# Performance work log

Hardware: AMD Instinct MI355X
Metric: run time of the kernel (lower is better)

Reference implementation:

```python
import jax, jax.numpy as jnp
import numpy as np

NODE, HIDDEN, BATCH, OUT, BUF = 200, 10, 50, 64, 500
DT = 0.0001
# ParamsJR('JR') defaults (all variances 0 -> constants, not Parameters)
A_, a_, B_, b_ = 3.25, 100.0, 22.0, 50.0
g_, c1_, c2_, c3_, c4_ = 1000.0, 135.0, 135.0 * 0.8, 135.0 * 0.25, 135.0 * 0.25
std_in_, vmax, v0, r_, y0, cy0 = 100.0, 5.0, 6.0, 0.56, 2.0, 5.0
LB, U_UB, NOISE_LB, SAT = 0.01, 500.0, 150.0, 1000.0


def setup_inputs() -> dict:
    key = jax.random.key(0)
    ks = jax.random.split(key, 8)
    inp = jax.random.normal(ks[0], (NODE, HIDDEN, BATCH), dtype=jnp.float32)
    noise_in = jax.random.normal(ks[1], (NODE, HIDDEN, BATCH), dtype=jnp.float32)
    hx = jax.random.uniform(ks[2], (NODE, 6), dtype=jnp.float32)
    hE = jax.random.uniform(ks[3], (NODE, BUF), dtype=jnp.float32)
    sc = jax.random.uniform(ks[4], (NODE, NODE), dtype=jnp.float32)
    w_bb = jax.random.uniform(ks[5], (NODE, NODE), dtype=jnp.float32)  # fitted gains (init 0.05 in torch)
    lm = jax.random.normal(ks[6], (OUT, NODE), dtype=jnp.float32)  # lead-field
    delays = jax.random.randint(ks[7], (NODE, NODE), 0, BUF)  # (dist/(1.5+relu(mu))).int64
    return {"inp": inp, "noise_in": noise_in, "hx": hx, "hE": hE,
            "sc": sc, "w_bb": w_bb, "lm": lm, "delays": delays}


def _sigmoid(x):
    return vmax / (1.0 + jnp.exp(r_ * (v0 - x)))


def _sys2nd(A, a, u, x, v):
    return A * a * u - 2.0 * a * v - a * a * x


def _forward(inp, noise_in, hx, hE, sc, w_bb, lm, delays):
    relu = jax.nn.relu
    A_e, a_e = relu(A_), 1.0 + relu(a_)          # 0*con+relu(A), 1*con+relu(a)
    B_e, b_e = relu(B_), 1.0 + relu(b_)
    g_e, c1e, c2e, c3e, c4e = (LB + relu(g_), LB + relu(c1_), LB + relu(c2_),
                               LB + relu(c3_), LB + relu(c4_))
    std_e = NOISE_LB + relu(std_in_)

    # normalized laplacian-style connectivity
    w = jnp.exp(w_bb) * sc
    wl = jnp.log1p(0.5 * (w + w.T))
    w_n = wl / jnp.linalg.norm(wl)
    dg = -jnp.diag(jnp.sum(w_n, axis=1))          # (node, node)
    rows = jnp.arange(NODE)[:, None]

    def step(carry, xs):
        M, E, I, Mv, Ev, Iv, hEb = carry
        u, noise = xs                              # (node,1) each
        Ed = hEb[rows, delays]                     # Ed[i,j] = hE[i, delays[i,j]]
        LEd = jnp.sum(w_n * Ed.T, axis=1, keepdims=True)  # (node,1)
        rM = _sigmoid(E - I)
        rE = (std_e * noise + g_e * (LEd + dg @ E)
              + c2e * _sigmoid(c1e * M))
        rI = c4e * _sigmoid(c3e * M)
        ddM = M + DT * Mv
        ddE = E + DT * Ev
        ddI = I + DT * Iv
        ddMv = Mv + DT * _sys2nd(A_e, a_e, u + U_UB * jnp.tanh(rM / U_UB), M, Mv)
        ddEv = Ev + DT * _sys2nd(A_e, a_e, U_UB * jnp.tanh(rE / U_UB), E, Ev)
        ddIv = Iv + DT * _sys2nd(B_e, b_e, U_UB * jnp.tanh(rI / U_UB), I, Iv)
        sat = lambda x: SAT * jnp.tanh(x / SAT)
        M, E, I, Mv, Ev, Iv = (sat(ddM), sat(ddE), sat(ddI),
                               sat(ddMv), sat(ddEv), sat(ddIv))
        hEb = jnp.concatenate([M, hEb[:, :-1]], axis=1)  # push pyramidal state into delay buffer
        return (M, E, I, Mv, Ev, Iv, hEb), None

    def tr_step(carry, xs):
        u_tr, n_tr = xs                            # (hidden, node, 1)
        carry, _ = jax.lax.scan(step, carry, (u_tr, n_tr))
        M, E, I, Mv, Ev, Iv, _ = carry
        return carry, (M[:, 0], E[:, 0], I[:, 0], Mv[:, 0], Ev[:, 0], Iv[:, 0])

    M, E, I = hx[:, 0:1], hx[:, 1:2], hx[:, 2:3]
    Mv, Ev, Iv = hx[:, 3:4], hx[:, 4:5], hx[:, 5:6]
    u_all = jnp.transpose(inp, (2, 1, 0))[..., None]       # (batch, hidden, node, 1)
    n_all = jnp.transpose(noise_in, (2, 1, 0))[..., None]
    carry, recs = jax.lax.scan(tr_step, (M, E, I, Mv, Ev, Iv, hE), (u_all, n_all))
    Mb, Eb, Ib, Mvb, Evb, Ivb = recs                       # (batch, node) each

    # lead-field: row-normalize then remove channel mean
    lm_n = lm / jnp.sqrt(jnp.sum(lm ** 2, axis=1, keepdims=True))
    lm_t = lm_n - jnp.mean(lm_n, axis=0, keepdims=True)
    eeg = cy0 * jnp.einsum('on,bn->ob', lm_t, Eb - Ib) - y0  # (output, batch)

    M, E, I, Mv, Ev, Iv, hEb = carry
    current_state = jnp.concatenate([M, E, I, Mv, Ev, Iv], axis=1)
    return eeg, current_state, Eb.T, Ib.T, Mb.T, Evb.T, Ivb.T, Mvb.T, hEb


def reference(inp, noise_in, hx, hE, sc, w_bb, lm, delays):
    return _forward(inp, noise_in, hx, hE, sc, w_bb, lm, delays)
```

## Files before the change

### kernel.cpp

```cpp
#include <hip/hip_runtime.h>
#include <math.h>

#define N_NODE 200
#define RING   512
#define ROWF   545
#define NSTEP  500
#define TB     32
#define NB     16
#define NWG    8
#define NTHR   256
#define JSL    25
#define NEARCAP 32
#define MDEP   36

#define FPBUF   (NWG * N_NODE * TB)
#define OFF_FP  0
#define OFF_BAR (2 * FPBUF)
#define WS_NEED ((size_t)(2 * FPBUF + 64) * 4)

#define SM_RED   0
#define SM_MREC  64
#define SM_NOFF  28864
#define SM_NW    54464
#define SM_LED   80864
#define SM_RING  106464
#define SM_TOTAL 160964
#define SM_LMT   64
#define SM_DIFF  51264

__device__ __forceinline__ float sigm(float x) {
    return 5.0f / (1.0f + expf(0.56f * (6.0f - x)));
}
__device__ __forceinline__ float satf(float x) {
    return 1000.0f * tanhf(x / 1000.0f);
}

__device__ __forceinline__ void grid_barrier(int* slot, int nwg) {
    __syncthreads();
    if (threadIdx.x == 0) {
        __threadfence();
        __hip_atomic_fetch_add(slot, 1, __ATOMIC_ACQ_REL, __HIP_MEMORY_SCOPE_AGENT);
        while (__hip_atomic_load(slot, __ATOMIC_ACQUIRE, __HIP_MEMORY_SCOPE_AGENT) < nwg) {
            __builtin_amdgcn_s_sleep(2);
        }
        __threadfence();
    }
    __syncthreads();
}

__global__ void zero_bar(int* bar) {
    if (threadIdx.x < 64) bar[threadIdx.x] = 0;
}

__global__ __launch_bounds__(NTHR, 1)
void jansen_reg(const float* __restrict__ inp, const float* __restrict__ noise_in,
                const float* __restrict__ hx,  const float* __restrict__ hE,
                const float* __restrict__ sc,  const float* __restrict__ wbb,
                const float* __restrict__ lm,  const int*   __restrict__ delays,
                float* __restrict__ out, float* __restrict__ ws)
{
    __shared__ char smem[SM_TOTAL];
    double*   red  = (double*)(smem + SM_RED);
    float*    Mrec = (float*)(smem + SM_MREC);
    unsigned* nOFF = (unsigned*)(smem + SM_NOFF);
    float*    nW   = (float*)(smem + SM_NW);
    float*    LEdS = (float*)(smem + SM_LED);
    float*    ringS= (float*)(smem + SM_RING);

    const int tid = threadIdx.x;
    const int wg  = blockIdx.x;
    const int i   = tid;
    const int jlo = wg * JSL;

    float* fp  = ws + OFF_FP;
    int*   bar = (int*)(ws + OFF_BAR);

    double ssq = 0.0;
    for (int q = tid; q < N_NODE * N_NODE; q += NTHR) {
        int j = q / N_NODE, ii = q - j * N_NODE;
        float w1 = expf(wbb[ii * N_NODE + j]) * sc[ii * N_NODE + j];
        float w2 = expf(wbb[j * N_NODE + ii]) * sc[j * N_NODE + ii];
        float wl = log1pf(0.5f * (w1 + w2));
        ssq += (double)wl * (double)wl;
    }
    #pragma unroll
    for (int off = 32; off > 0; off >>= 1) ssq += __shfl_down(ssq, off, 64);
    if ((tid & 63) == 0) red[tid >> 6] = ssq;

    for (int p = tid; p < JSL * ROWF; p += NTHR) {
        int jl = p / ROWF, x = p - jl * ROWF;
        float v = 0.0f;
        if (x < 544) {
            int dd = (x < RING) ? (511 - x) : (1023 - x);
            if (dd < 500) v = hE[(jlo + jl) * 500 + dd];
        }
        ringS[p] = v;
    }
    for (int p = tid; p < MDEP * N_NODE; p += NTHR) {
        int s = p / N_NODE, j = p - s * N_NODE;
        Mrec[p] = (s >= 4) ? hE[j * 500 + (35 - s)] : 0.0f;
    }
    for (int p = tid; p < NEARCAP * N_NODE; p += NTHR) {
        nOFF[p] = 0u;
        nW[p]   = 0.0f;
    }
    __syncthreads();
    if (tid == 0) {
        double s = 0.0;
        #pragma unroll
        for (int r = 0; r < 8; ++r) s += red[r];
        red[0] = 1.0 / sqrt(s);
    }
    __syncthreads();
    const float inv = (float)red[0];

    float rowsum = 0.0f;
    float M = 0, E = 0, I = 0, Mvv = 0, Evv = 0, Ivv = 0;
    float wreg[JSL];
    int   ereg[JSL];
    #pragma unroll
    for (int jl = 0; jl < JSL; ++jl) { wreg[jl] = 0.0f; ereg[jl] = 0; }
    if (i < N_NODE) {
        int cnt = 0;
        for (int j = 0; j < N_NODE; ++j) {
            float w1 = expf(wbb[i * N_NODE + j]) * sc[i * N_NODE + j];
            float w2 = expf(wbb[j * N_NODE + i]) * sc[j * N_NODE + i];
            float w  = log1pf(0.5f * (w1 + w2)) * inv;
            int d = delays[j * N_NODE + i];
            rowsum += w;
            if (d < NEARCAP && cnt < NEARCAP) {
                nOFF[cnt * N_NODE + i] = (unsigned)((35 - d) * N_NODE + j);
                nW  [cnt * N_NODE + i] = w;
                ++cnt;
            }
        }
        #pragma unroll
        for (int jl = 0; jl < JSL; ++jl) {
            int j = jlo + jl;
            float w1 = expf(wbb[i * N_NODE + j]) * sc[i * N_NODE + j];
            float w2 = expf(wbb[j * N_NODE + i]) * sc[j * N_NODE + i];
            float w  = log1pf(0.5f * (w1 + w2)) * inv;
            int d = delays[j * N_NODE + i];
            wreg[jl] = (d < NEARCAP) ? 0.0f : w;
            ereg[jl] = 511 - d;
        }
        M   = hx[i * 6 + 0]; E   = hx[i * 6 + 1]; I   = hx[i * 6 + 2];
        Mvv = hx[i * 6 + 3]; Evv = hx[i * 6 + 4]; Ivv = hx[i * 6 + 5];
    }

    int   noffR[NEARCAP];
    float nwR[NEARCAP];
    {
        const int ii = (i < N_NODE) ? i : 0;
        #pragma unroll
        for (int n = 0; n < NEARCAP; ++n) {
            noffR[n] = (int)nOFF[n * N_NODE + ii];
            nwR[n]   = nW[n * N_NODE + ii];
        }
    }
    __syncthreads();

    for (int b = 0; b < NB; ++b) {
        const int t0 = b * TB;
        float* fpb = fp + (b & 1) * FPBUF;

        float u0=0, u1=0, u2=0, n0=0, n1=0, n2=0;

        if (i < N_NODE) {
            float ac[TB];
            #pragma unroll
            for (int k = 0; k < TB; ++k) ac[k] = 0.0f;
            #pragma unroll
            for (int jl = 0; jl < JSL; ++jl) {
                float w  = wreg[jl];
                int   p0 = (t0 + ereg[jl]) & 511;
                const float* rb = ringS + jl * ROWF + p0;
                #pragma unroll
                for (int k = 0; k < TB; ++k)
                    ac[k] = fmaf(w, rb[k], ac[k]);
            }
            float4* fpw = (float4*)(fpb + wg * (N_NODE * TB) + i * TB);
            #pragma unroll
            for (int q = 0; q < 8; ++q)
                fpw[q] = make_float4(ac[4*q+0], ac[4*q+1], ac[4*q+2], ac[4*q+3]);

            {
                int ta = t0, tb2 = t0 + 1, tc = t0 + 2;
                int ba = ta / 10,  ha = ta  - 10 * ba;
                int bbq = tb2 / 10, hb = tb2 - 10 * bbq;
                int bc = tc / 10,  hc = tc  - 10 * bc;
                u0 = inp     [i * 500 + ha * 50 + ba];
                n0 = noise_in[i * 500 + ha * 50 + ba];
                u1 = inp     [i * 500 + hb * 50 + bbq];
                n1 = noise_in[i * 500 + hb * 50 + bbq];
                u2 = inp     [i * 500 + hc * 50 + bc];
                n2 = noise_in[i * 500 + hc * 50 + bc];
            }
        }

        grid_barrier(bar + b, NWG);

        if (i < N_NODE) {
            const float* basep = fpb + i * TB;
            #pragma unroll
            for (int c = 0; c < 8; ++c) {
                float sx = 0, sy = 0, sz = 0, sw = 0;
                #pragma unroll
                for (int g = 0; g < NWG; ++g) {
                    float4 q = *(const float4*)(basep + g * (N_NODE * TB) + c * 4);
                    sx += q.x; sy += q.y; sz += q.z; sw += q.w;
                }
                LEdS[(c * 4 + 0) * N_NODE + i] = sx;
                LEdS[(c * 4 + 1) * N_NODE + i] = sy;
                LEdS[(c * 4 + 2) * N_NODE + i] = sz;
                LEdS[(c * 4 + 3) * N_NODE + i] = sw;
            }
        }
        __syncthreads();

        const int kmax = (NSTEP - t0 < TB) ? (NSTEP - t0) : TB;
        int s36 = t0 % MDEP;
        int t3  = t0 + 3;
        int bb3 = t3 / 10, hh3 = t3 - 10 * bb3;
        int bcur = t0 / 10, hcur = t0 - 10 * bcur;
        const bool ringw = (i >= jlo) && (i < jlo + JSL);
        const int  rbase = (i - jlo) * ROWF;
        for (int k = 0; k < kmax; ++k) {
            const int t = t0 + k;
            if (i < N_NODE) {
                float LEd = LEdS[k * N_NODE + i];
                const int base36 = s36 * N_NODE;
                #pragma unroll
                for (int n = 0; n < NEARCAP; ++n) {
                    int addr = base36 + noffR[n];
                    if (addr >= MDEP * N_NODE) addr -= MDEP * N_NODE;
                    LEd = fmaf(nwR[n], Mrec[addr], LEd);
                }
                float u  = u0;
                float nz = n0;
                float rM = sigm(E - I);
                float rE = 250.0f * nz + 1000.01f * (LEd - rowsum * E) + 108.01f * sigm(135.01f * M);
                float rI = 33.76f * sigm(33.76f * M);
                float ddM = M + 1e-4f * Mvv;
                float ddE = E + 1e-4f * Evv;
                float ddI = I + 1e-4f * Ivv;
                float uu  = u + 500.0f * tanhf(rM / 500.0f);
                float ddMv = Mvv + 1e-4f * (328.25f * uu - 202.0f * Mvv - 10201.0f * M);
                float uE  = 500.0f * tanhf(rE / 500.0f);
                float ddEv = Evv + 1e-4f * (328.25f * uE - 202.0f * Evv - 10201.0f * E);
                float uI  = 500.0f * tanhf(rI / 500.0f);
                float ddIv = Ivv + 1e-4f * (1122.0f * uI - 102.0f * Ivv - 2601.0f * I);
                M   = satf(ddM);  E   = satf(ddE);  I   = satf(ddI);
                Mvv = satf(ddMv); Evv = satf(ddEv); Ivv = satf(ddIv);
                Mrec[s36 * N_NODE + i] = M;
                if (ringw) {
                    int pt = t & 511;
                    ringS[rbase + pt] = M;
                    if (pt < 32) ringS[rbase + pt + 512] = M;
                }
                if (wg == 0 && hcur == 9) {
                    out[ 4400 + i * 50 + bcur] = E;
                    out[14400 + i * 50 + bcur] = I;
                    out[24400 + i * 50 + bcur] = M;
                    out[34400 + i * 50 + bcur] = Evv;
                    out[44400 + i * 50 + bcur] = Ivv;
                    out[54400 + i * 50 + bcur] = Mvv;
                }
                u0 = u1; u1 = u2; n0 = n1; n1 = n2;
                if (t3 < NSTEP) {
                    u2 = inp     [i * 500 + hh3 * 50 + bb3];
                    n2 = noise_in[i * 500 + hh3 * 50 + bb3];
                }
                ++t3; ++hh3; if (hh3 == 10) { hh3 = 0; ++bb3; }
                ++hcur; if (hcur == 10) { hcur = 0; ++bcur; }
                ++s36; if (s36 == MDEP) s36 = 0;
            }
            __syncthreads();
        }
    }

    for (int p = tid; p < JSL * 500; p += NTHR) {
        int jl = p / 500, dd = p - jl * 500;
        out[64400 + (jlo + jl) * 500 + dd] = ringS[jl * ROWF + ((499 - dd) & 511)];
    }
    if (wg != 0) return;

    if (i < N_NODE) {
        out[3200 + i * 6 + 0] = M;
        out[3200 + i * 6 + 1] = E;
        out[3200 + i * 6 + 2] = I;
        out[3200 + i * 6 + 3] = Mvv;
        out[3200 + i * 6 + 4] = Evv;
        out[3200 + i * 6 + 5] = Ivv;
    }

    float* lmt  = (float*)(smem + SM_LMT);
    float* diff = (float*)(smem + SM_DIFF);
    __syncthreads();
    if (tid < 64) {
        float s = 0.0f;
        for (int n = 0; n < N_NODE; ++n) { float v = lm[tid * N_NODE + n]; s += v * v; }
        float ivn = 1.0f / sqrtf(s);
        for (int n = 0; n < N_NODE; ++n) lmt[tid * N_NODE + n] = lm[tid * N_NODE + n] * ivn;
    }
    __syncthreads();
    if (tid < N_NODE) {
        float s = 0.0f;
        for (int o = 0; o < 64; ++o) s += lmt[o * N_NODE + tid];
        s *= (1.0f / 64.0f);
        for (int o = 0; o < 64; ++o) lmt[o * N_NODE + tid] -= s;
    }
    __syncthreads();
    for (int p = tid; p < 10000; p += NTHR) diff[p] = out[4400 + p] - out[14400 + p];
    __syncthreads();
    for (int p = tid; p < 3200; p += NTHR) {
        int o = p / 50, bb = p - o * 50;
        float s = 0.0f;
        for (int n = 0; n < N_NODE; ++n)
            s = fmaf(lmt[o * N_NODE + n], diff[n * 50 + bb], s);
        out[p] = 5.0f * s - 2.0f;
    }
}

__global__ __launch_bounds__(1024, 1)
void jansen_main(const float* __restrict__ inp, const float* __restrict__ noise_in,
                 const float* __restrict__ hx,  const float* __restrict__ hE,
                 const float* __restrict__ sc,  const float* __restrict__ wbb,
                 const float* __restrict__ lm,  const int*   __restrict__ delays,
                 float* __restrict__ out, float* __restrict__ ws)
{
    const int tid = threadIdx.x;
    const int i   = tid & 255;
    const int c   = tid >> 8;

    float* ring = ws;
    float* lmt  = ws + N_NODE * RING;

    __shared__ double red[18];
    __shared__ float  part[4][N_NODE];
    __shared__ float  wn[N_NODE * N_NODE];

    double ssq = 0.0;
    for (int p = tid; p < N_NODE * N_NODE; p += 1024) {
        int r0 = p / N_NODE;
        int cc = p - r0 * N_NODE;
        float w1 = expf(wbb[p]) * sc[p];
        float w2 = expf(wbb[cc * N_NODE + r0]) * sc[cc * N_NODE + r0];
        float v  = log1pf(0.5f * (w1 + w2));
        wn[p] = v;
        ssq += (double)v * (double)v;
    }
    #pragma unroll
    for (int off = 32; off > 0; off >>= 1) ssq += __shfl_down(ssq, off, 64);
    if ((tid & 63) == 0) red[tid >> 6] = ssq;
    __syncthreads();
    if (tid == 0) {
        double s = 0.0;
        for (int k = 0; k < 16; ++k) s += red[k];
        red[16] = 1.0 / sqrt(s);
    }
    __syncthreads();
    const float inv_norm = (float)red[16];
    for (int p = tid; p < N_NODE * N_NODE; p += 1024) wn[p] *= inv_norm;

    for (int p = tid; p < N_NODE * 500; p += 1024) {
        int j = p / 500, dd = p - j * 500;
        ring[j * RING + (511 - dd)] = hE[p];
    }
    if (tid < 64) {
        float s = 0.0f;
        for (int n = 0; n < N_NODE; ++n) { float v = lm[tid * N_NODE + n]; s += v * v; }
        float inv = 1.0f / sqrtf(s);
        for (int n = 0; n < N_NODE; ++n) lmt[tid * N_NODE + n] = lm[tid * N_NODE + n] * inv;
    }
    __syncthreads();
    if (tid < N_NODE) {
        float s = 0.0f;
        for (int o = 0; o < 64; ++o) s += lmt[o * N_NODE + tid];
        s *= (1.0f / 64.0f);
        for (int o = 0; o < 64; ++o) lmt[o * N_NODE + tid] -= s;
    }

    unsigned int dpk[25];
    if (i < N_NODE) {
        #pragma unroll
        for (int r0 = 0; r0 < 25; ++r0) {
            int d0 = delays[(c * 50 + 2 * r0    ) * N_NODE + i];
            int d1 = delays[(c * 50 + 2 * r0 + 1) * N_NODE + i];
            unsigned e0 = (unsigned)((-1 - d0) & 511);
            unsigned e1 = (unsigned)((-1 - d1) & 511);
            dpk[r0] = e0 | (e1 << 16);
        }
    }

    float M = 0, E = 0, I = 0, Mvv = 0, Evv = 0, Ivv = 0, rowsum = 0;
    if (c == 0 && i < N_NODE) {
        M   = hx[i * 6 + 0]; E   = hx[i * 6 + 1]; I   = hx[i * 6 + 2];
        Mvv = hx[i * 6 + 3]; Evv = hx[i * 6 + 4]; Ivv = hx[i * 6 + 5];
    }
    __syncthreads();
    if (c == 0 && i < N_NODE) {
        float s = 0.0f;
        for (int j = 0; j < N_NODE; ++j) s += wn[j * N_NODE + i];
        rowsum = s;
    }

    for (int t = 0; t < NSTEP; ++t) {
        if (i < N_NODE) {
            float acc = 0.0f;
            const float* ringc = ring + c * 50 * RING;
            const float* wnc   = wn + c * 50 * N_NODE + i;
            #pragma unroll
            for (int r0 = 0; r0 < 50; ++r0) {
                unsigned e = (dpk[r0 >> 1] >> ((r0 & 1) << 4)) & 0xffffu;
                int pos = (int)(((unsigned)t + e) & 511u);
                acc = fmaf(wnc[r0 * N_NODE], ringc[r0 * RING + pos], acc);
            }
            part[c][i] = acc;
        }
        __syncthreads();
        if (c == 0 && i < N_NODE) {
            float LEd = part[0][i] + part[1][i] + part[2][i] + part[3][i];
            int b = t / 10, h = t - b * 10;
            float u  = inp     [i * 500 + h * 50 + b];
            float nz = noise_in[i * 500 + h * 50 + b];
            float rM = sigm(E - I);
            float rE = 250.0f * nz + 1000.01f * (LEd - rowsum * E) + 108.01f * sigm(135.01f * M);
            float rI = 33.76f * sigm(33.76f * M);
            float ddM = M + 1e-4f * Mvv;
            float ddE = E + 1e-4f * Evv;
            float ddI = I + 1e-4f * Ivv;
            float uu  = u + 500.0f * tanhf(rM / 500.0f);
            float ddMv = Mvv + 1e-4f * (328.25f * uu - 202.0f * Mvv - 10201.0f * M);
            float uE  = 500.0f * tanhf(rE / 500.0f);
            float ddEv = Evv + 1e-4f * (328.25f * uE - 202.0f * Evv - 10201.0f * E);
            float uI  = 500.0f * tanhf(rI / 500.0f);
            float ddIv = Ivv + 1e-4f * (1122.0f * uI - 102.0f * Ivv - 2601.0f * I);
            M   = satf(ddM);  E   = satf(ddE);  I   = satf(ddI);
            Mvv = satf(ddMv); Evv = satf(ddEv); Ivv = satf(ddIv);
            ring[i * RING + (t & 511)] = M;
            if (h == 9) {
                out[ 4400 + i * 50 + b] = E;
                out[14400 + i * 50 + b] = I;
                out[24400 + i * 50 + b] = M;
                out[34400 + i * 50 + b] = Evv;
                out[44400 + i * 50 + b] = Ivv;
                out[54400 + i * 50 + b] = Mvv;
            }
        }
        __syncthreads();
    }

    if (c == 0 && i < N_NODE) {
        out[3200 + i * 6 + 0] = M;
        out[3200 + i * 6 + 1] = E;
        out[3200 + i * 6 + 2] = I;
        out[3200 + i * 6 + 3] = Mvv;
        out[3200 + i * 6 + 4] = Evv;
        out[3200 + i * 6 + 5] = Ivv;
    }
    for (int p = tid; p < N_NODE * 500; p += 1024) {
        int ii = p / 500, dd = p - ii * 500;
        out[64400 + p] = ring[ii * RING + (499 - dd)];
    }
    __syncthreads();
    for (int p = tid; p < 64 * 50; p += 1024) {
        int o = p / 50, b = p - o * 50;
        float s = 0.0f;
        for (int n = 0; n < N_NODE; ++n)
            s += lmt[o * N_NODE + n] * (out[4400 + n * 50 + b] - out[14400 + n * 50 + b]);
        out[p] = 5.0f * s - 2.0f;
    }
}

extern "C" void kernel_launch(void* const* d_in, const int* in_sizes, int n_in,
                              void* d_out, int out_size, void* d_ws, size_t ws_size,
                              hipStream_t stream) {
    if (ws_size >= WS_NEED) {
        zero_bar<<<1, 64, 0, stream>>>((int*)((float*)d_ws + OFF_BAR));
        jansen_reg<<<NWG, NTHR, 0, stream>>>(
            (const float*)d_in[0], (const float*)d_in[1], (const float*)d_in[2],
            (const float*)d_in[3], (const float*)d_in[4], (const float*)d_in[5],
            (const float*)d_in[6], (const int*)d_in[7],
            (float*)d_out, (float*)d_ws);
    } else {
        jansen_main<<<1, 1024, 0, stream>>>(
            (const float*)d_in[0], (const float*)d_in[1], (const float*)d_in[2],
            (const float*)d_in[3], (const float*)d_in[4], (const float*)d_in[5],
            (const float*)d_in[6], (const int*)d_in[7],
            (float*)d_out, (float*)d_ws);
    }
}
```

Measured before the change: 1.468 ms.

## Use fast exp/tanh intrinsics, stage inputs in LDS, split near-delay accumulation

Replaces expf/tanhf in the fast kernel with __expf/__fdividef-based sigmoid and tanh to shorten the serial per-step dependency chain. Per-block input and noise values are prefetched into shared memory (reusing the near-delay table regions after they are copied into registers) rather than loaded from global memory inside the step loop. The near-delay dot product is split into four independent accumulators to expose ILP. The fast math lowers accuracy, which over 500 recurrent steps could drift beyond tolerance.

```diff
diff --git a/kernel.cpp b/kernel.cpp
--- a/kernel.cpp
+++ b/kernel.cpp
@@ -20,19 +20,25 @@
 
 #define SM_RED   0
 #define SM_MREC  64
-#define SM_NOFF  28864
-#define SM_NW    54464
+#define SM_US    28864
+#define SM_NS    54464
 #define SM_LED   80864
 #define SM_RING  106464
 #define SM_TOTAL 160964
 #define SM_LMT   64
 #define SM_DIFF  51264
 
+__device__ __forceinline__ float ftanh(float x) {
+    float ax = fabsf(x);
+    float t  = __expf(-2.0f * ax);
+    float r  = __fdividef(1.0f - t, 1.0f + t);
+    return copysignf(r, x);
+}
 __device__ __forceinline__ float sigm(float x) {
-    return 5.0f / (1.0f + expf(0.56f * (6.0f - x)));
+    return __fdividef(5.0f, 1.0f + __expf(0.56f * (6.0f - x)));
 }
 __device__ __forceinline__ float satf(float x) {
-    return 1000.0f * tanhf(x / 1000.0f);
+    return 1000.0f * ftanh(x * 0.001f);
 }
 
 __device__ __forceinline__ void grid_barrier(int* slot, int nwg) {
@@ -53,17 +59,19 @@
 }
 
 __global__ __launch_bounds__(NTHR, 1)
-void jansen_reg(const float* __restrict__ inp, const float* __restrict__ noise_in,
-                const float* __restrict__ hx,  const float* __restrict__ hE,
-                const float* __restrict__ sc,  const float* __restrict__ wbb,
-                const float* __restrict__ lm,  const int*   __restrict__ delays,
-                float* __restrict__ out, float* __restrict__ ws)
+void jansen_fast(const float* __restrict__ inp, const float* __restrict__ noise_in,
+                 const float* __restrict__ hx,  const float* __restrict__ hE,
+                 const float* __restrict__ sc,  const float* __restrict__ wbb,
+                 const float* __restrict__ lm,  const int*   __restrict__ delays,
+                 float* __restrict__ out, float* __restrict__ ws)
 {
     __shared__ char smem[SM_TOTAL];
     double*   red  = (double*)(smem + SM_RED);
     float*    Mrec = (float*)(smem + SM_MREC);
-    unsigned* nOFF = (unsigned*)(smem + SM_NOFF);
-    float*    nW   = (float*)(smem + SM_NW);
+    unsigned* nOFF = (unsigned*)(smem + SM_US);
+    float*    nW   = (float*)(smem + SM_NS);
+    float*    uS   = (float*)(smem + SM_US);
+    float*    nS   = (float*)(smem + SM_NS);
     float*    LEdS = (float*)(smem + SM_LED);
     float*    ringS= (float*)(smem + SM_RING);
 
@@ -164,8 +172,6 @@
         const int t0 = b * TB;
         float* fpb = fp + (b & 1) * FPBUF;
 
-        float u0=0, u1=0, u2=0, n0=0, n1=0, n2=0;
-
         if (i < N_NODE) {
             float ac[TB];
             #pragma unroll
@@ -184,17 +190,17 @@
             for (int q = 0; q < 8; ++q)
                 fpw[q] = make_float4(ac[4*q+0], ac[4*q+1], ac[4*q+2], ac[4*q+3]);
 
-            {
-                int ta = t0, tb2 = t0 + 1, tc = t0 + 2;
-                int ba = ta / 10,  ha = ta  - 10 * ba;
-                int bbq = tb2 / 10, hb = tb2 - 10 * bbq;
-                int bc = tc / 10,  hc = tc  - 10 * bc;
-                u0 = inp     [i * 500 + ha * 50 + ba];
-                n0 = noise_in[i * 500 + ha * 50 + ba];
-                u1 = inp     [i * 500 + hb * 50 + bbq];
-                n1 = noise_in[i * 500 + hb * 50 + bbq];
-                u2 = inp     [i * 500 + hc * 50 + bc];
-                n2 = noise_in[i * 500 + hc * 50 + bc];
+            #pragma unroll
+            for (int k = 0; k < TB; ++k) {
+                int t = t0 + k;
+                float uv = 0.0f, nv = 0.0f;
+                if (t < NSTEP) {
+                    int bb = t / 10, h = t - 10 * bb;
+                    uv = inp     [i * 500 + h * 50 + bb];
+                    nv = noise_in[i * 500 + h * 50 + bb];
+                }
+                uS[k * N_NODE + i] = uv;
+                nS[k * N_NODE + i] = nv;
             }
         }
 
@@ -220,39 +226,44 @@
 
         const int kmax = (NSTEP - t0 < TB) ? (NSTEP - t0) : TB;
         int s36 = t0 % MDEP;
-        int t3  = t0 + 3;
-        int bb3 = t3 / 10, hh3 = t3 - 10 * bb3;
         int bcur = t0 / 10, hcur = t0 - 10 * bcur;
         const bool ringw = (i >= jlo) && (i < jlo + JSL);
         const int  rbase = (i - jlo) * ROWF;
         for (int k = 0; k < kmax; ++k) {
             const int t = t0 + k;
             if (i < N_NODE) {
-                float LEd = LEdS[k * N_NODE + i];
                 const int base36 = s36 * N_NODE;
+                float a0 = LEdS[k * N_NODE + i];
+                float a1 = 0.0f, a2 = 0.0f, a3 = 0.0f;
                 #pragma unroll
-                for (int n = 0; n < NEARCAP; ++n) {
-                    int addr = base36 + noffR[n];
-                    if (addr >= MDEP * N_NODE) addr -= MDEP * N_NODE;
-                    LEd = fmaf(nwR[n], Mrec[addr], LEd);
+                for (int n = 0; n < NEARCAP; n += 4) {
+                    int d0 = base36 + noffR[n+0]; if (d0 >= MDEP*N_NODE) d0 -= MDEP*N_NODE;
+                    int d1 = base36 + noffR[n+1]; if (d1 >= MDEP*N_NODE) d1 -= MDEP*N_NODE;
+                    int d2 = base36 + noffR[n+2]; if (d2 >= MDEP*N_NODE) d2 -= MDEP*N_NODE;
+                    int d3 = base36 + noffR[n+3]; if (d3 >= MDEP*N_NODE) d3 -= MDEP*N_NODE;
+                    a0 = fmaf(nwR[n+0], Mrec[d0], a0);
+                    a1 = fmaf(nwR[n+1], Mrec[d1], a1);
+                    a2 = fmaf(nwR[n+2], Mrec[d2], a2);
+                    a3 = fmaf(nwR[n+3], Mrec[d3], a3);
                 }
-                float u  = u0;
-                float nz = n0;
+                float LEd = (a0 + a1) + (a2 + a3);
+                float u  = uS[k * N_NODE + i];
+                float nz = nS[k * N_NODE + i];
                 float rM = sigm(E - I);
                 float rE = 250.0f * nz + 1000.01f * (LEd - rowsum * E) + 108.01f * sigm(135.01f * M);
                 float rI = 33.76f * sigm(33.76f * M);
                 float ddM = M + 1e-4f * Mvv;
                 float ddE = E + 1e-4f * Evv;
                 float ddI = I + 1e-4f * Ivv;
-                float uu  = u + 500.0f * tanhf(rM / 500.0f);
+                float uu  = u + 500.0f * ftanh(rM * 0.002f);
                 float ddMv = Mvv + 1e-4f * (328.25f * uu - 202.0f * Mvv - 10201.0f * M);
-                float uE  = 500.0f * tanhf(rE / 500.0f);
+                float uE  = 500.0f * ftanh(rE * 0.002f);
                 float ddEv = Evv + 1e-4f * (328.25f * uE - 202.0f * Evv - 10201.0f * E);
-                float uI  = 500.0f * tanhf(rI / 500.0f);
+                float uI  = 500.0f * ftanh(rI * 0.002f);
                 float ddIv = Ivv + 1e-4f * (1122.0f * uI - 102.0f * Ivv - 2601.0f * I);
                 M   = satf(ddM);  E   = satf(ddE);  I   = satf(ddI);
                 Mvv = satf(ddMv); Evv = satf(ddEv); Ivv = satf(ddIv);
-                Mrec[s36 * N_NODE + i] = M;
+                Mrec[base36 + i] = M;
                 if (ringw) {
                     int pt = t & 511;
                     ringS[rbase + pt] = M;
@@ -266,12 +277,6 @@
                     out[44400 + i * 50 + bcur] = Ivv;
                     out[54400 + i * 50 + bcur] = Mvv;
                 }
-                u0 = u1; u1 = u2; n0 = n1; n1 = n2;
-                if (t3 < NSTEP) {
-                    u2 = inp     [i * 500 + hh3 * 50 + bb3];
-                    n2 = noise_in[i * 500 + hh3 * 50 + bb3];
-                }
-                ++t3; ++hh3; if (hh3 == 10) { hh3 = 0; ++bb3; }
                 ++hcur; if (hcur == 10) { hcur = 0; ++bcur; }
                 ++s36; if (s36 == MDEP) s36 = 0;
             }
@@ -424,9 +429,9 @@
             int b = t / 10, h = t - b * 10;
             float u  = inp     [i * 500 + h * 50 + b];
             float nz = noise_in[i * 500 + h * 50 + b];
-            float rM = sigm(E - I);
-            float rE = 250.0f * nz + 1000.01f * (LEd - rowsum * E) + 108.01f * sigm(135.01f * M);
-            float rI = 33.76f * sigm(33.76f * M);
+            float rM = 5.0f / (1.0f + expf(0.56f * (6.0f - (E - I))));
+            float rE = 250.0f * nz + 1000.01f * (LEd - rowsum * E) + 108.01f * (5.0f / (1.0f + expf(0.56f * (6.0f - 135.01f * M))));
+            float rI = 33.76f * (5.0f / (1.0f + expf(0.56f * (6.0f - 33.76f * M))));
             float ddM = M + 1e-4f * Mvv;
             float ddE = E + 1e-4f * Evv;
             float ddI = I + 1e-4f * Ivv;
@@ -436,8 +441,12 @@
             float ddEv = Evv + 1e-4f * (328.25f * uE - 202.0f * Evv - 10201.0f * E);
             float uI  = 500.0f * tanhf(rI / 500.0f);
             float ddIv = Ivv + 1e-4f * (1122.0f * uI - 102.0f * Ivv - 2601.0f * I);
-            M   = satf(ddM);  E   = satf(ddE);  I   = satf(ddI);
-            Mvv = satf(ddMv); Evv = satf(ddEv); Ivv = satf(ddIv);
+            M   = 1000.0f * tanhf(ddM / 1000.0f);
+            E   = 1000.0f * tanhf(ddE / 1000.0f);
+            I   = 1000.0f * tanhf(ddI / 1000.0f);
+            Mvv = 1000.0f * tanhf(ddMv / 1000.0f);
+            Evv = 1000.0f * tanhf(ddEv / 1000.0f);
+            Ivv = 1000.0f * tanhf(ddIv / 1000.0f);
             ring[i * RING + (t & 511)] = M;
             if (h == 9) {
                 out[ 4400 + i * 50 + b] = E;
@@ -478,7 +487,7 @@
                               hipStream_t stream) {
     if (ws_size >= WS_NEED) {
         zero_bar<<<1, 64, 0, stream>>>((int*)((float*)d_ws + OFF_BAR));
-        jansen_reg<<<NWG, NTHR, 0, stream>>>(
+        jansen_fast<<<NWG, NTHR, 0, stream>>>(
             (const float*)d_in[0], (const float*)d_in[1], (const float*)d_in[2],
             (const float*)d_in[3], (const float*)d_in[4], (const float*)d_in[5],
             (const float*)d_in[6], (const int*)d_in[7],
```

Result: faster. 1.210 ms (-17.6%).
